# Performance work log

Measured on AMD Instinct MI355X. Metric: run time of the kernel, lower is better.

## Reference

```python
import jax, jax.numpy as jnp
import numpy as np

IMG = 224      # image_size
P = 16         # patch_size
HP = P // 2    # half_patch
D = 768        # projection_dim
C_IN = 3
B = 64


def setup_inputs() -> dict:
    key = jax.random.key(0)
    k1, k2 = jax.random.split(key, 2)
    images = jax.random.normal(k1, (B, IMG, IMG, C_IN), dtype=jnp.float32)
    pvs = P * P * C_IN * 5  # patch_vector_size with 5-way channel concat
    W = jax.random.normal(k2, (pvs, D), dtype=jnp.float32) * 0.02
    b = jnp.zeros((D,), dtype=jnp.float32)
    return {"images": images, "W": W, "b": b}


def _crop_shift_pad(images, oh, ow):
    # Faithful to the TF code: crop at (oh, ow) then pad back at the SAME
    # (oh, ow) -> identity inside the region, zeros on the complementary border.
    th = IMG - HP
    tw = IMG - HP
    out = jnp.zeros_like(images)
    return out.at[:, oh:oh + th, ow:ow + tw, :].set(images[:, oh:oh + th, ow:ow + tw, :])


def reference(images, W, b):
    # 4 shifted-pad variants: left-up, left-down, right-up, right-down
    offsets = [(0, 0), (HP, 0), (0, HP), (HP, HP)]
    concat = jnp.concatenate(
        [images] + [_crop_shift_pad(images, oh, ow) for oh, ow in offsets],
        axis=-1)  # (B, IMG, IMG, 5*C_IN)
    Bn, _, _, C = concat.shape
    g = IMG // P  # grid size = 14
    # tf.image.extract_patches with stride==size, VALID: non-overlapping patches,
    # patch contents row-major with channel fastest -> reshape/transpose.
    x = concat.reshape(Bn, g, P, g, P, C)
    x = x.transpose(0, 1, 3, 2, 4, 5).reshape(Bn, g * g, P * P * C)  # (B, 196, 3840)
    return x @ W + b  # (B, 196, 768)
```

## Files before the change

kernel.cpp:

```cpp
#include <hip/hip_runtime.h>
#include <hip/hip_bf16.h>

typedef _Float16 half8 __attribute__((ext_vector_type(8)));
typedef _Float16 half4 __attribute__((ext_vector_type(4)));
typedef float floatx4 __attribute__((ext_vector_type(4)));

#define PD 768
#define KE 768
#define NB 64

__device__ __forceinline__ int cls_row_base(int cls) {
  return (cls == 0) ? 0 : (cls == 1) ? 64 : (cls == 2) ? 832 : (cls == 3) ? 896
       : (cls == 4) ? 1664 : (cls == 5) ? 10880 : (cls == 6) ? 11648
       : (cls == 7) ? 11712 : 12480;
}

__device__ __forceinline__ void gl_lds16(const _Float16* g, _Float16* l) {
  __builtin_amdgcn_global_load_lds(
      (const __attribute__((address_space(1))) unsigned int*)g,
      (__attribute__((address_space(3))) unsigned int*)l, 16, 0, 0);
}

__global__ __launch_bounds__(256) void prep_all(
    const float* __restrict__ W, const float* __restrict__ img,
    _Float16* __restrict__ Weff, _Float16* __restrict__ Ap) {
  __shared__ float Wl[60][68];
  const int t = threadIdx.x;

  if (blockIdx.x < 768) {
    const int ck = blockIdx.x & 63;
    const int cd = blockIdx.x >> 6;
    const int p0 = ck * 4;
    const int d0 = cd * 64;
    for (int c = t; c < 960; c += 256) {
      int row = c >> 4, off = (c & 15) * 4;
      *(floatx4*)&Wl[row][off] =
          *(const floatx4*)&W[(size_t)(p0 * 15 + row) * PD + d0 + off];
    }
    __syncthreads();
    if (t < 192) {
      int d = t / 3, q = t - (t / 3) * 3;
      float vout[9][4];
#pragma unroll
      for (int s = 0; s < 4; ++s) {
        int kl = q * 4 + s;
        int pl = kl / 3, cc = kl - pl * 3;
        int pix = p0 + pl;
        int ph = pix >> 4, pw = pix & 15;
        int rb = pl * 15 + cc;
        float w0 = Wl[rb][d],     w1 = Wl[rb + 3][d], w2 = Wl[rb + 6][d],
              w3 = Wl[rb + 9][d], w4 = Wl[rb + 12][d];
        float hlt[3] = {1.f, 1.f, (ph < 8) ? 1.f : 0.f};
        float hge[3] = {(ph >= 8) ? 1.f : 0.f, 1.f, 1.f};
        float wlt[3] = {1.f, 1.f, (pw < 8) ? 1.f : 0.f};
        float wge[3] = {(pw >= 8) ? 1.f : 0.f, 1.f, 1.f};
#pragma unroll
        for (int rh = 0; rh < 3; ++rh)
#pragma unroll
          for (int rw = 0; rw < 3; ++rw)
            vout[rh * 3 + rw][s] = w0 + hlt[rh] * wlt[rw] * w1
                + hge[rh] * wlt[rw] * w2 + hlt[rh] * wge[rw] * w3
                + hge[rh] * wge[rw] * w4;
      }
#pragma unroll
      for (int cls = 0; cls < 9; ++cls) {
        half4 h;
        h.x = (_Float16)vout[cls][0]; h.y = (_Float16)vout[cls][1];
        h.z = (_Float16)vout[cls][2]; h.w = (_Float16)vout[cls][3];
        *(half4*)&Weff[((size_t)cls * PD + d0 + d) * KE + ck * 12 + q * 4] = h;
      }
    }
  } else {
    const int total = NB * 224 * 84;
    for (int id = (blockIdx.x - 768) * 256 + t; id < total; id += 2048 * 256) {
      int b   = id / 18816;
      int rem = id - b * 18816;
      int h   = rem / 84;
      int c8  = rem - h * 84;
      int gw  = c8 / 6;
      int j8  = c8 - gw * 6;
      int gh  = h >> 4, ph = h & 15;
      int rh  = (gh == 0) ? 0 : ((gh >= 13) ? 2 : 1);
      int rw  = (gw == 0) ? 0 : ((gw >= 13) ? 2 : 1);
      int gh0 = (rh == 1) ? 1 : ((rh == 2) ? 13 : 0);
      int gw0 = (rw == 1) ? 1 : ((rw == 2) ? 13 : 0);
      int nh  = (rh == 1) ? 12 : 1;
      int nw  = (rw == 1) ? 12 : 1;
      int cls = rh * 3 + rw;
      int r   = cls_row_base(cls) + (b * nh + (gh - gh0)) * nw + (gw - gw0);
      const float* src = img + (size_t)(b * 224 + h) * 672 + c8 * 8;
      floatx4 v0 = *(const floatx4*)src;
      floatx4 v1 = *(const floatx4*)(src + 4);
      half8 o;
      o[0] = (_Float16)v0.x; o[1] = (_Float16)v0.y;
      o[2] = (_Float16)v0.z; o[3] = (_Float16)v0.w;
      o[4] = (_Float16)v1.x; o[5] = (_Float16)v1.y;
      o[6] = (_Float16)v1.z; o[7] = (_Float16)v1.w;
      *(half8*)&Ap[(size_t)r * KE + ph * 48 + j8 * 8] = o;
    }
  }
}

#define BM 128
#define BN 128

__global__ __launch_bounds__(256) void spt_gemm(
    const _Float16* __restrict__ Ap, const _Float16* __restrict__ Weff,
    const float* __restrict__ bias, float* __restrict__ out) {
  __shared__ _Float16 Al[2][BM * 64];
  __shared__ _Float16 Bl[2][BN * 64];

  const int t = threadIdx.x;
  const int wid = (blockIdx.x & 7) * 75 + (blockIdx.x >> 3);
  const int nt = wid % 6;
  const int bt = wid / 6;

  int cls, mt;
  if      (bt < 1)  { cls = 0; mt = bt; }
  else if (bt < 7)  { cls = 1; mt = bt - 1; }
  else if (bt < 8)  { cls = 2; mt = bt - 7; }
  else if (bt < 14) { cls = 3; mt = bt - 8; }
  else if (bt < 86) { cls = 4; mt = bt - 14; }
  else if (bt < 92) { cls = 5; mt = bt - 86; }
  else if (bt < 93) { cls = 6; mt = bt - 92; }
  else if (bt < 99) { cls = 7; mt = bt - 93; }
  else              { cls = 8; mt = bt - 99; }

  const int rh  = cls / 3, rw = cls % 3;
  const int per = ((rh == 1) ? 12 : 1) * ((rw == 1) ? 12 : 1);
  const int Mc  = NB * per;
  const int cbase   = cls_row_base(cls);
  const int rowbase = cbase + mt * BM;

  const int w = t >> 6, lane = t & 63;
  const int wr = w >> 1, wc = w & 1;
  const int lrow = lane & 15, lq = lane >> 4;

  const int srow = t >> 3;
  const int js = (t & 7) ^ (srow & 7);
  const _Float16* Agp[4];
  const _Float16* Bgp[4];
#pragma unroll
  for (int i = 0; i < 4; ++i) {
    int rA = rowbase + i * 32 + srow;
    int rmax = cbase + Mc - 1;
    rA = (rA > rmax) ? rmax : rA;
    Agp[i] = Ap + (size_t)rA * KE + js * 8;
    Bgp[i] = Weff + ((size_t)cls * PD + nt * BN + i * 32 + srow) * KE + js * 8;
  }

  floatx4 acc[4][4];
#pragma unroll
  for (int m = 0; m < 4; ++m)
#pragma unroll
    for (int n = 0; n < 4; ++n) acc[m][n] = (floatx4)0.f;

#define STAGE(ks, sel)                                                        \
  {                                                                           \
    _Pragma("unroll")                                                         \
    for (int i = 0; i < 4; ++i)                                               \
      gl_lds16(Agp[i] + (ks) * 64, &Al[sel][i * 2048 + w * 512]);             \
    _Pragma("unroll")                                                         \
    for (int i = 0; i < 4; ++i)                                               \
      gl_lds16(Bgp[i] + (ks) * 64, &Bl[sel][i * 2048 + w * 512]);             \
  }

  int cur = 0;
  STAGE(0, 0);
  __syncthreads();
  for (int ks = 0; ks < 12; ++ks) {
    if (ks < 11) STAGE(ks + 1, cur ^ 1);
#pragma unroll
    for (int kf = 0; kf < 2; ++kf) {
      half8 af[4], bf[4];
#pragma unroll
      for (int m = 0; m < 4; ++m) {
        int row = wr * 64 + m * 16 + lrow;
        af[m] = *(const half8*)&Al[cur][row * 64
                 + ((kf * 32 + lq * 8) ^ ((row & 7) * 8))];
      }
#pragma unroll
      for (int n = 0; n < 4; ++n) {
        int row = wc * 64 + n * 16 + lrow;
        bf[n] = *(const half8*)&Bl[cur][row * 64
                 + ((kf * 32 + lq * 8) ^ ((row & 7) * 8))];
      }
#pragma unroll
      for (int m = 0; m < 4; ++m)
#pragma unroll
        for (int n = 0; n < 4; ++n)
          acc[m][n] = __builtin_amdgcn_mfma_f32_16x16x32_f16(
              af[m], bf[n], acc[m][n], 0, 0, 0);
    }
    __syncthreads();
    cur ^= 1;
  }

  const int gh0 = (rh == 1) ? 1 : ((rh == 2) ? 13 : 0);
  const int gw0 = (rw == 1) ? 1 : ((rw == 2) ? 13 : 0);
  const int nw  = (rw == 1) ? 12 : 1;

  const int col = nt * BN + wc * 64 + lrow;
  float bv[4];
#pragma unroll
  for (int n = 0; n < 4; ++n) bv[n] = bias[col + n * 16];
  const int rq = lq * 4;
#pragma unroll
  for (int m = 0; m < 4; ++m) {
#pragma unroll
    for (int j = 0; j < 4; ++j) {
      int R = rowbase + wr * 64 + m * 16 + rq + j;
      int r = R - cbase;
      if (r < Mc) {
        int b, ih, iw;
        if (per == 1)        { b = r; ih = 0; iw = 0; }
        else if (per == 12)  { b = r / 12; int rm = r - b * 12;
                               ih = (nw == 1) ? rm : 0; iw = (nw == 1) ? 0 : rm; }
        else                 { b = r / 144; int rm = r - b * 144;
                               ih = rm / 12; iw = rm - ih * 12; }
        int p = (gh0 + ih) * 14 + (gw0 + iw);
        float* orow = out + ((size_t)b * 196 + p) * PD + col;
#pragma unroll
        for (int n = 0; n < 4; ++n) orow[n * 16] = acc[m][n][j] + bv[n];
      }
    }
  }
}

extern "C" void kernel_launch(void* const* d_in, const int* in_sizes, int n_in,
                              void* d_out, int out_size, void* d_ws, size_t ws_size,
                              hipStream_t stream) {
  const float* img  = (const float*)d_in[0];
  const float* W    = (const float*)d_in[1];
  const float* bias = (const float*)d_in[2];
  float* out = (float*)d_out;
  _Float16* Weff = (_Float16*)d_ws;
  _Float16* Ap   = (_Float16*)((char*)d_ws + 10616832);

  prep_all<<<2816, 256, 0, stream>>>(W, img, Weff, Ap);
  spt_gemm<<<600, 256, 0, stream>>>(Ap, Weff, bias, out);
}
```

Before: 135.6 us.

## Split K-tile into half-phases with fine-grained vmcnt waits and MFMA priority

Restructures the GEMM main loop so each 64-wide K step is staged as two 32-wide halves in separate LDS buffers, with per-warp row ownership of loads. Each phase waits only on its own outstanding global-to-LDS loads via s_waitcnt vmcnt, uses a raw s_barrier, reads fragments, then issues the next half's prefetch before running MFMAs under raised priority. Fragment offsets and the XOR swizzle are precomputed. The goal is finer-grained overlap of loads with compute and fewer full barriers. The hand-written vmcnt counts depend on exact instruction ordering, so a compiler reordering could break correctness.

```diff
diff --git a/kernel.cpp b/kernel.cpp
--- a/kernel.cpp
+++ b/kernel.cpp
@@ -107,8 +107,8 @@
 __global__ __launch_bounds__(256) void spt_gemm(
     const _Float16* __restrict__ Ap, const _Float16* __restrict__ Weff,
     const float* __restrict__ bias, float* __restrict__ out) {
-  __shared__ _Float16 Al[2][BM * 64];
-  __shared__ _Float16 Bl[2][BN * 64];
+  __shared__ _Float16 Al[2][2][4096];
+  __shared__ _Float16 Bl[2][2][4096];
 
   const int t = threadIdx.x;
   const int wid = (blockIdx.x & 7) * 75 + (blockIdx.x >> 3);
@@ -136,18 +136,29 @@
   const int wr = w >> 1, wc = w & 1;
   const int lrow = lane & 15, lq = lane >> 4;
 
-  const int srow = t >> 3;
-  const int js = (t & 7) ^ (srow & 7);
-  const _Float16* Agp[4];
-  const _Float16* Bgp[4];
-#pragma unroll
-  for (int i = 0; i < 4; ++i) {
-    int rA = rowbase + i * 32 + srow;
+  const int srow = lane >> 2;
+  const int js = (lane & 3) ^ (srow & 3);
+  const _Float16* Agp[2];
+  const _Float16* Bgp[2];
+#pragma unroll
+  for (int i = 0; i < 2; ++i) {
+    int rA = rowbase + i * 64 + w * 16 + srow;
     int rmax = cbase + Mc - 1;
     rA = (rA > rmax) ? rmax : rA;
     Agp[i] = Ap + (size_t)rA * KE + js * 8;
-    Bgp[i] = Weff + ((size_t)cls * PD + nt * BN + i * 32 + srow) * KE + js * 8;
-  }
+    Bgp[i] = Weff + ((size_t)cls * PD + nt * BN + i * 64 + w * 16 + srow) * KE
+             + js * 8;
+  }
+  const int ldsb = (w * 16) * 32;
+
+  const int cswz = (lq ^ (lrow & 3)) * 8;
+  int aoff[4], boff[4];
+#pragma unroll
+  for (int m = 0; m < 4; ++m)
+    aoff[m] = (wr * 64 + m * 16 + lrow) * 32 + cswz;
+#pragma unroll
+  for (int n = 0; n < 4; ++n)
+    boff[n] = (wc * 64 + n * 16 + lrow) * 32 + cswz;
 
   floatx4 acc[4][4];
 #pragma unroll
@@ -155,44 +166,44 @@
 #pragma unroll
     for (int n = 0; n < 4; ++n) acc[m][n] = (floatx4)0.f;
 
-#define STAGE(ks, sel)                                                        \
+#define ISSUE_HALF(ks, sel, h)                                                \
   {                                                                           \
     _Pragma("unroll")                                                         \
-    for (int i = 0; i < 4; ++i)                                               \
-      gl_lds16(Agp[i] + (ks) * 64, &Al[sel][i * 2048 + w * 512]);             \
-    _Pragma("unroll")                                                         \
-    for (int i = 0; i < 4; ++i)                                               \
-      gl_lds16(Bgp[i] + (ks) * 64, &Bl[sel][i * 2048 + w * 512]);             \
-  }
-
+    for (int i = 0; i < 2; ++i) {                                             \
+      gl_lds16(Agp[i] + (ks) * 64 + (h) * 32, &Al[sel][h][ldsb + i * 2048]);  \
+      gl_lds16(Bgp[i] + (ks) * 64 + (h) * 32, &Bl[sel][h][ldsb + i * 2048]);  \
+    }                                                                         \
+  }
+
+#define PHASE(ks, curb, h, last)                                              \
+  {                                                                           \
+    if (last) asm volatile("s_waitcnt vmcnt(0)" ::: "memory");                \
+    else      asm volatile("s_waitcnt vmcnt(4)" ::: "memory");                \
+    __builtin_amdgcn_s_barrier();                                             \
+    half8 af[4], bf[4];                                                       \
+    _Pragma("unroll")                                                         \
+    for (int m = 0; m < 4; ++m)                                               \
+      af[m] = *(const half8*)&Al[curb][h][aoff[m]];                           \
+    _Pragma("unroll")                                                         \
+    for (int n = 0; n < 4; ++n)                                               \
+      bf[n] = *(const half8*)&Bl[curb][h][boff[n]];                           \
+    if ((ks) < 11) ISSUE_HALF((ks) + 1, (curb) ^ 1, h);                       \
+    __builtin_amdgcn_s_setprio(1);                                            \
+    _Pragma("unroll")                                                         \
+    for (int m = 0; m < 4; ++m)                                               \
+      _Pragma("unroll")                                                       \
+      for (int n = 0; n < 4; ++n)                                             \
+        acc[m][n] = __builtin_amdgcn_mfma_f32_16x16x32_f16(                   \
+            af[m], bf[n], acc[m][n], 0, 0, 0);                                \
+    __builtin_amdgcn_s_setprio(0);                                            \
+  }
+
+  ISSUE_HALF(0, 0, 0);
+  ISSUE_HALF(0, 0, 1);
   int cur = 0;
-  STAGE(0, 0);
-  __syncthreads();
   for (int ks = 0; ks < 12; ++ks) {
-    if (ks < 11) STAGE(ks + 1, cur ^ 1);
-#pragma unroll
-    for (int kf = 0; kf < 2; ++kf) {
-      half8 af[4], bf[4];
-#pragma unroll
-      for (int m = 0; m < 4; ++m) {
-        int row = wr * 64 + m * 16 + lrow;
-        af[m] = *(const half8*)&Al[cur][row * 64
-                 + ((kf * 32 + lq * 8) ^ ((row & 7) * 8))];
-      }
-#pragma unroll
-      for (int n = 0; n < 4; ++n) {
-        int row = wc * 64 + n * 16 + lrow;
-        bf[n] = *(const half8*)&Bl[cur][row * 64
-                 + ((kf * 32 + lq * 8) ^ ((row & 7) * 8))];
-      }
-#pragma unroll
-      for (int m = 0; m < 4; ++m)
-#pragma unroll
-        for (int n = 0; n < 4; ++n)
-          acc[m][n] = __builtin_amdgcn_mfma_f32_16x16x32_f16(
-              af[m], bf[n], acc[m][n], 0, 0, 0);
-    }
-    __syncthreads();
+    PHASE(ks, cur, 0, false);
+    PHASE(ks, cur, 1, ks == 11);
     cur ^= 1;
   }
 
```

Measured after the change: 136.7 us. No clear change (+0.8%).
